# Optimization experiments

Measured on AMD Instinct MI355X. Metric: run time of the kernel, lower is better.

## Reference

```python
import jax, jax.numpy as jnp
import numpy as np

N, D, H1, K = 4096, 128, 256, 128


def setup_inputs() -> dict:
    key = jax.random.key(0)
    ks = jax.random.split(key, 8)
    A = jax.random.uniform(ks[3], (D, D), dtype=jnp.float32)
    A = A * (1.0 - jnp.eye(D, dtype=jnp.float32))  # DAG prob mask, no self-loops
    return {
        "x": jax.random.normal(ks[0], (N, D), dtype=jnp.float32),
        "weight": jax.random.normal(ks[1], (D, D), dtype=jnp.float32) * 0.1,
        "bias": jax.random.normal(ks[2], (1, D), dtype=jnp.float32) * 0.1,
        "A": A,
        "W1": jax.random.normal(ks[4], (D, H1), dtype=jnp.float32) * 0.1,
        "b1": jax.random.normal(ks[5], (H1,), dtype=jnp.float32) * 0.1,
        "W2": jax.random.normal(ks[6], (H1, K), dtype=jnp.float32) * 0.1,
        "b2": jax.random.normal(ks[7], (K,), dtype=jnp.float32) * 0.1,
    }


def reference(x, weight, bias, A, W1, b1, W2, b2):
    # to_adj (eval path): masked weights
    W = weight * A                                   # [D, D]
    y = x @ W + bias                                 # [N, D]
    # __expand__ builds diag(y[n]) [N,D,D]; since e[n,i,:] = y[n,i]*I[i,:],
    # the first Linear collapses to a per-row scaling of W1 (same math, fused):
    # e @ W1 -> y[n,i] * W1[i,:]
    h1 = jax.nn.relu(y[:, :, None] * W1[None, :, :] + b1)   # [N, D, H1]
    f = (h1 @ W2 + b2).sum(axis=2)                   # [N, D] (sum over output dim)
    # h_func, method='gnn'
    I = jnp.eye(D, dtype=x.dtype)
    A2 = jnp.square(W)
    M = I + A2 / D
    E = jnp.linalg.matrix_power(M, D - 1)
    h_val = (E.T * M).sum() - D
    # l1_reg (same prob mask in eval)
    reg = jnp.abs(W).sum()
    return (f, h_val, reg)
```

## Files before the change

### kernel.cpp

```cpp
#include <hip/hip_runtime.h>

#define NN 4096
#define DD 128
#define HH1 256

#define WS_S    0
#define WS_S2   16384
#define WS_S3   32768
#define WS_S4   49152
#define WS_W    65536
#define WS_W2S  81920
#define WS_PAIR 82176
#define WS_B2S  82688
#define WS_TACC 82696
#define WS_DONE 82708
#define WS_REGP 82712
#define WS_XT   82944
#define WS_YT   607232
#define WS_REQ_FLOATS 1131520
#define WS_REQ_BYTES  (WS_REQ_FLOATS * 4UL)

#define O_S    0
#define O_S2   16384
#define O_S3   32768
#define O_S4   49152
#define O_W2S  65536
#define O_B2S  65792
#define O_TACC 65808
#define O_DONE 65824
#define O_REGP 65840

__device__ __forceinline__ float waveReduce(float v) {
#pragma unroll
  for (int off = 32; off > 0; off >>= 1) v += __shfl_down(v, off, 64);
  return v;
}


__global__ __launch_bounds__(256) void kA2(
    const float* __restrict__ weight, const float* __restrict__ Amat,
    const float* __restrict__ W2, const float* __restrict__ b2,
    const float* __restrict__ b1v, const float* __restrict__ x,
    float* __restrict__ ws) {
  const int b = blockIdx.x, tid = threadIdx.x;
  __shared__ float s_lds[DD * DD];
  __shared__ float xs[128 * 133];
  if (b < 64) {
    const float4* w4 = (const float4*)weight;
    const float4* a4 = (const float4*)Amat;
    float4* s4 = (float4*)s_lds;
    const float inv = 1.0f / 128.0f;
    for (int e = tid; e < DD * DD / 4; e += 256) {
      float4 wv = w4[e], av = a4[e], o;
      float t;
      t = wv.x * av.x; o.x = t * t * inv;
      t = wv.y * av.y; o.y = t * t * inv;
      t = wv.z * av.z; o.z = t * t * inv;
      t = wv.w * av.w; o.w = t * t * inv;
      s4[e] = o;
    }
    __syncthreads();
    const int i = (b << 1) + (tid >> 7), j = tid & 127;
    const float* row = &s_lds[i * DD];
    float acc = 0.f;
#pragma unroll 8
    for (int k = 0; k < DD; ++k) acc = fmaf(row[k], s_lds[k * DD + j], acc);
    ws[WS_S2 + i * DD + j] = acc;
  } else if (b < 72) {
    const int base = (b - 64) * 2048;
    const float inv = 1.0f / 128.0f;
    for (int e = tid; e < 2048; e += 256) {
      const int idx = base + e;
      const float w = weight[idx] * Amat[idx];
      ws[WS_W + idx] = w;
      ws[WS_S + idx] = w * w * inv;
    }
  } else if (b == 72) {
    const float4* r = (const float4*)(W2 + tid * 128);
    float4 s4 = make_float4(0.f, 0.f, 0.f, 0.f);
#pragma unroll 8
    for (int k = 0; k < 32; ++k) {
      const float4 v = r[k];
      s4.x += v.x; s4.y += v.y; s4.z += v.z; s4.w += v.w;
    }
    const float w2sv = (s4.x + s4.y) + (s4.z + s4.w);
    ws[WS_W2S + tid] = w2sv;
    ((float2*)(ws + WS_PAIR))[tid] = make_float2(b1v[tid], w2sv);
  } else if (b == 73) {
    __shared__ float red[4];
    float v = (tid < 128) ? b2[tid] : 0.f;
    v = waveReduce(v);
    if ((tid & 63) == 0) red[tid >> 6] = v;
    __syncthreads();
    if (tid == 0) ws[WS_B2S] = (red[0] + red[1]) + (red[2] + red[3]);
    if (tid >= 64 && tid < 74) ws[WS_TACC + (tid - 64)] = 0.f;
    if (tid == 96) *(unsigned int*)(ws + WS_DONE) = 0u;
  } else if (b < 82) {
    const int bb = b - 74;
    const int base = bb * 2048;
    float s = 0.f;
    for (int e = tid; e < 2048; e += 256) {
      const int idx = base + e;
      s += fabsf(weight[idx] * Amat[idx]);
    }
    s = waveReduce(s);
    __shared__ float red2[4];
    if ((tid & 63) == 0) red2[tid >> 6] = s;
    __syncthreads();
    if (tid == 0) ws[WS_REGP + bb] = (red2[0] + red2[1]) + (red2[2] + red2[3]);
  } else {
    const int n0 = (b - 82) * 128;
    const float4* x4 = (const float4*)x;
    for (int e = tid; e < 4096; e += 256) {
      const int r = e >> 5, c = e & 31;
      const float4 v = x4[(n0 + r) * 32 + c];
      float* p = &xs[r * 133 + (c << 2)];
      p[0] = v.x; p[1] = v.y; p[2] = v.z; p[3] = v.w;
    }
    __syncthreads();
    float* xT = ws + WS_XT;
    const int c = tid & 31, ks = tid >> 5;
#pragma unroll 4
    for (int m = 0; m < 16; ++m) {
      const int k = ks + (m << 3);
      float4 o;
      o.x = xs[((c << 2) + 0) * 133 + k];
      o.y = xs[((c << 2) + 1) * 133 + k];
      o.z = xs[((c << 2) + 2) * 133 + k];
      o.w = xs[((c << 2) + 3) * 133 + k];
      *(float4*)&xT[k * NN + n0 + (c << 2)] = o;
    }
  }
}

__global__ __launch_bounds__(256) void kB2(const float* __restrict__ bias,
                                           float* __restrict__ ws) {
  const int tid = threadIdx.x;
  if (blockIdx.x < 128) {
    const int sb = blockIdx.x;
    const bool isS4 = sb >= 64;
    const int mb = isS4 ? sb - 64 : sb;
    const float* __restrict__ L = ws + WS_S2;
    const float* __restrict__ R = ws + (isS4 ? WS_S2 : WS_S);
    float* __restrict__ O = ws + (isS4 ? WS_S4 : WS_S3);
    const int i = (mb << 1) + (tid >> 7), j = tid & 127;
    float acc = 0.f;
#pragma unroll 8
    for (int k = 0; k < DD; ++k) acc = fmaf(L[i * DD + k], R[k * DD + j], acc);
    O[i * DD + j] = acc;
    return;
  }
  const int kb = blockIdx.x - 128;
  const int n0 = (kb & 15) << 8, i0 = (kb >> 4) << 3;
  const int n = n0 + tid;
  const float* __restrict__ xT = ws + WS_XT;
  const float* __restrict__ Wm = ws + WS_W;
  float* __restrict__ yT = ws + WS_YT;
  float acc[8];
#pragma unroll
  for (int q = 0; q < 8; ++q) acc[q] = 0.f;
#pragma unroll 8
  for (int k = 0; k < DD; ++k) {
    const float xv = xT[k * NN + n];
    const float* Wk = Wm + k * DD + i0;
#pragma unroll
    for (int q = 0; q < 8; ++q) acc[q] = fmaf(Wk[q], xv, acc[q]);
  }
#pragma unroll
  for (int q = 0; q < 8; ++q) yT[(i0 + q) * NN + n] = acc[q] + bias[i0 + q];
}

__global__ __launch_bounds__(256) void kC2(const float* __restrict__ W1,
                                           float* __restrict__ ws,
                                           float* __restrict__ out) {
  const int tid = threadIdx.x;
  if (blockIdx.x < 512) {
    __shared__ float ts[256 * 5];
    const int fb = blockIdx.x;
    const int n0 = (fb >> 5) << 8, i0 = (fb & 31) << 2;
    const int w = tid >> 6, l = tid & 63;
    const int iu = __builtin_amdgcn_readfirstlane(i0 + w);
    const float* __restrict__ yT = ws + WS_YT;
    float t[4];
#pragma unroll
    for (int q = 0; q < 4; ++q) t[q] = yT[iu * NN + n0 + (q << 6) + l];
    const float sb2 = ws[WS_B2S];
    float acc[4];
#pragma unroll
    for (int q = 0; q < 4; ++q) acc[q] = sb2;
    const float* __restrict__ W1row = W1 + iu * HH1;
    const float2* __restrict__ pr = (const float2*)(ws + WS_PAIR);
#pragma unroll 8
    for (int j = 0; j < HH1; ++j) {
      const float sw1 = W1row[j];
      const float2 p = pr[j];
      const float vb = p.x;
#pragma unroll
      for (int q = 0; q < 4; ++q) {
        const float h = fmaxf(fmaf(t[q], sw1, vb), 0.f);
        acc[q] = fmaf(h, p.y, acc[q]);
      }
    }
#pragma unroll
    for (int q = 0; q < 4; ++q) ts[((q << 6) + l) * 5 + w] = acc[q];
    __syncthreads();
    const int m = tid;
    float4 o;
    o.x = ts[m * 5 + 0]; o.y = ts[m * 5 + 1];
    o.z = ts[m * 5 + 2]; o.w = ts[m * 5 + 3];
    *(float4*)&out[(n0 + m) * DD + i0] = o;
    return;
  }
  const int tb = blockIdx.x - 512;
  const int i = (tb << 1) + (tid >> 7), j = tid & 127;
  const float* S1 = ws + WS_S;
  const float* S2 = ws + WS_S2;
  const float* S3 = ws + WS_S3;
  const float* S4 = ws + WS_S4;
  const float a1 = S1[i * DD + j], a2 = S2[i * DD + j], a3 = S3[i * DD + j];
  const float b1t = S1[j * DD + i], b2t = S2[j * DD + i],
              b3t = S3[j * DD + i], b4t = S4[j * DD + i];
  float e7 = 0.f;
#pragma unroll 8
  for (int k = 0; k < DD; ++k) e7 = fmaf(S3[i * DD + k], S4[k * DD + j], e7);
  float c[10];
  c[0] = a1 * b1t; c[1] = a2 * b1t; c[2] = a2 * b2t; c[3] = a3 * b2t;
  c[4] = a3 * b3t; c[5] = a3 * b4t; c[6] = e7 * b1t; c[7] = e7 * b2t;
  c[8] = e7 * b3t; c[9] = e7 * b4t;
  __shared__ float red[4][10];
#pragma unroll
  for (int m = 0; m < 10; ++m) {
    const float v = waveReduce(c[m]);
    if ((tid & 63) == 0) red[tid >> 6][m] = v;
  }
  __syncthreads();
  if (tid == 0) {
    float* tacc = ws + WS_TACC;
    for (int m = 0; m < 10; ++m)
      atomicAdd(&tacc[m], (red[0][m] + red[1][m]) + (red[2][m] + red[3][m]));
    __threadfence();
    unsigned int* done = (unsigned int*)(ws + WS_DONE);
    const unsigned int old = atomicAdd(done, 1u);
    if (old == 63u) {
      __threadfence();
      double h = 0.0, C = 8128.0;
      for (int kk = 2; kk <= 11; ++kk) {
        const float tv = atomicAdd(&tacc[kk - 2], 0.0f);
        h += C * (double)tv;
        C = C * (double)(128 - kk) / (double)(kk + 1);
      }
      float reg = 0.f;
      for (int m = 0; m < 8; ++m) reg += ws[WS_REGP + m];
      out[NN * DD] = (float)h;
      out[NN * DD + 1] = reg;
    }
  }
}

__global__ __launch_bounds__(256) void kA_old(
    const float* __restrict__ weight, const float* __restrict__ Amat,
    const float* __restrict__ W2, const float* __restrict__ b2,
    float* __restrict__ ws) {
  const int b = blockIdx.x, tid = threadIdx.x;
  if (b < 64) {
    __shared__ float s_lds[DD * DD];
    const float4* w4 = (const float4*)weight;
    const float4* a4 = (const float4*)Amat;
    float4* s4 = (float4*)s_lds;
    const float inv = 1.0f / 128.0f;
    for (int e = tid; e < DD * DD / 4; e += 256) {
      float4 wv = w4[e], av = a4[e], o;
      float t;
      t = wv.x * av.x; o.x = t * t * inv;
      t = wv.y * av.y; o.y = t * t * inv;
      t = wv.z * av.z; o.z = t * t * inv;
      t = wv.w * av.w; o.w = t * t * inv;
      s4[e] = o;
    }
    __syncthreads();
    const int i = (b << 1) + (tid >> 7), j = tid & 127;
    const float* row = &s_lds[i * DD];
    float acc = 0.f;
#pragma unroll 8
    for (int k = 0; k < DD; ++k) acc = fmaf(row[k], s_lds[k * DD + j], acc);
    ws[O_S2 + i * DD + j] = acc;
  } else if (b < 72) {
    const int base = (b - 64) * 2048;
    const float inv = 1.0f / 128.0f;
    for (int e = tid; e < 2048; e += 256) {
      const int idx = base + e;
      const float w = weight[idx] * Amat[idx];
      ws[O_S + idx] = w * w * inv;
    }
  } else if (b == 72) {
    const float4* r = (const float4*)(W2 + tid * 128);
    float4 s4 = make_float4(0.f, 0.f, 0.f, 0.f);
#pragma unroll 8
    for (int k = 0; k < 32; ++k) {
      const float4 v = r[k];
      s4.x += v.x; s4.y += v.y; s4.z += v.z; s4.w += v.w;
    }
    ws[O_W2S + tid] = (s4.x + s4.y) + (s4.z + s4.w);
  } else if (b == 73) {
    __shared__ float red[4];
    float v = (tid < 128) ? b2[tid] : 0.f;
    v = waveReduce(v);
    if ((tid & 63) == 0) red[tid >> 6] = v;
    __syncthreads();
    if (tid == 0) ws[O_B2S] = (red[0] + red[1]) + (red[2] + red[3]);
    if (tid >= 64 && tid < 74) ws[O_TACC + (tid - 64)] = 0.f;
    if (tid == 96) *(unsigned int*)(ws + O_DONE) = 0u;
  } else {
    const int bb = b - 74;
    const int base = bb * 2048;
    float s = 0.f;
    for (int e = tid; e < 2048; e += 256) {
      const int idx = base + e;
      s += fabsf(weight[idx] * Amat[idx]);
    }
    s = waveReduce(s);
    __shared__ float red[4];
    if ((tid & 63) == 0) red[tid >> 6] = s;
    __syncthreads();
    if (tid == 0) ws[O_REGP + bb] = (red[0] + red[1]) + (red[2] + red[3]);
  }
}

__global__ __launch_bounds__(256) void kB_old(
    const float* __restrict__ x, const float* __restrict__ weight,
    const float* __restrict__ Amat, const float* __restrict__ bias,
    const float* __restrict__ W1, const float* __restrict__ b1v,
    float* __restrict__ ws, float* __restrict__ out) {
  const int tid = threadIdx.x;
  if (blockIdx.x < 128) {
    const int sb = blockIdx.x;
    const bool isS4 = sb >= 64;
    const int mb = isS4 ? sb - 64 : sb;
    const float* __restrict__ L = ws + O_S2;
    const float* __restrict__ R = ws + (isS4 ? O_S2 : O_S);
    float* __restrict__ O = ws + (isS4 ? O_S4 : O_S3);
    const int i = (mb << 1) + (tid >> 7), j = tid & 127;
    float acc = 0.f;
#pragma unroll 8
    for (int k = 0; k < DD; ++k) acc = fmaf(L[i * DD + k], R[k * DD + j], acc);
    O[i * DD + j] = acc;
    return;
  }
  __shared__ float xs[64 * 132];
  __shared__ float4 fq[4 * 256];
  __shared__ float wcol[4 * 128];
  __shared__ float ts[64 * 5];
  const int fb = blockIdx.x - 128;
  const int i0 = (fb & 31) << 2, n0 = (fb >> 5) << 6;
  const float4* x4 = (const float4*)x;
  for (int e = tid; e < 64 * 32; e += 256) {
    const int r = e >> 5, c = e & 31;
    *(float4*)&xs[r * 132 + (c << 2)] = x4[(n0 + r) * 32 + c];
  }
  for (int e = tid; e < 512; e += 256) {
    const int w = e >> 7, k = e & 127;
    const int gi = k * DD + i0 + w;
    wcol[(w << 7) + k] = weight[gi] * Amat[gi];
  }
  const float* w2s = ws + O_W2S;
  for (int e = tid; e < 1024; e += 256) {
    const int w = e >> 8, j = e & 255;
    fq[(w << 8) + j] = make_float4(W1[(i0 + w) * HH1 + j], b1v[j], w2s[j], 0.f);
  }
  __syncthreads();
  const int w = tid >> 6, l = tid & 63;
  float t = bias[i0 + w];
  const float4* xr = (const float4*)&xs[l * 132];
  const float4* wc = (const float4*)&wcol[w << 7];
#pragma unroll
  for (int k = 0; k < 32; ++k) {
    const float4 xv = xr[k], wv = wc[k];
    t = fmaf(xv.x, wv.x, t);
    t = fmaf(xv.y, wv.y, t);
    t = fmaf(xv.z, wv.z, t);
    t = fmaf(xv.w, wv.w, t);
  }
  float acc = ws[O_B2S];
  const float4* fp = &fq[w << 8];
#pragma unroll 8
  for (int j = 0; j < HH1; ++j) {
    const float4 c = fp[j];
    acc = fmaf(fmaxf(fmaf(t, c.x, c.y), 0.f), c.z, acc);
  }
  ts[l * 5 + w] = acc;
  __syncthreads();
  if (tid < 64) {
    const float4 o = make_float4(ts[tid * 5 + 0], ts[tid * 5 + 1],
                                 ts[tid * 5 + 2], ts[tid * 5 + 3]);
    *(float4*)&out[(n0 + tid) * DD + i0] = o;
  }
}

__global__ __launch_bounds__(256) void kC_old(float* __restrict__ ws,
                                              float* __restrict__ out) {
  const int tid = threadIdx.x;
  const int i = (blockIdx.x << 1) + (tid >> 7), j = tid & 127;
  const float* S1 = ws + O_S;
  const float* S2 = ws + O_S2;
  const float* S3 = ws + O_S3;
  const float* S4 = ws + O_S4;
  const float a1 = S1[i * DD + j], a2 = S2[i * DD + j], a3 = S3[i * DD + j];
  const float b1t = S1[j * DD + i], b2t = S2[j * DD + i],
              b3t = S3[j * DD + i], b4t = S4[j * DD + i];
  float e7 = 0.f;
#pragma unroll 8
  for (int k = 0; k < DD; ++k) e7 = fmaf(S3[i * DD + k], S4[k * DD + j], e7);
  float c[10];
  c[0] = a1 * b1t; c[1] = a2 * b1t; c[2] = a2 * b2t; c[3] = a3 * b2t;
  c[4] = a3 * b3t; c[5] = a3 * b4t; c[6] = e7 * b1t; c[7] = e7 * b2t;
  c[8] = e7 * b3t; c[9] = e7 * b4t;
  __shared__ float red[4][10];
#pragma unroll
  for (int m = 0; m < 10; ++m) {
    const float v = waveReduce(c[m]);
    if ((tid & 63) == 0) red[tid >> 6][m] = v;
  }
  __syncthreads();
  if (tid == 0) {
    float* tacc = ws + O_TACC;
    for (int m = 0; m < 10; ++m)
      atomicAdd(&tacc[m], (red[0][m] + red[1][m]) + (red[2][m] + red[3][m]));
    __threadfence();
    unsigned int* done = (unsigned int*)(ws + O_DONE);
    const unsigned int old = atomicAdd(done, 1u);
    if (old == 63u) {
      __threadfence();
      double h = 0.0, C = 8128.0;
      for (int kk = 2; kk <= 11; ++kk) {
        const float tv = atomicAdd(&tacc[kk - 2], 0.0f);
        h += C * (double)tv;
        C = C * (double)(128 - kk) / (double)(kk + 1);
      }
      float reg = 0.f;
      for (int m = 0; m < 8; ++m) reg += ws[O_REGP + m];
      out[NN * DD] = (float)h;
      out[NN * DD + 1] = reg;
    }
  }
}

extern "C" void kernel_launch(void* const* d_in, const int* in_sizes, int n_in,
                              void* d_out, int out_size, void* d_ws,
                              size_t ws_size, hipStream_t stream) {
  const float* x      = (const float*)d_in[0];
  const float* weight = (const float*)d_in[1];
  const float* bias   = (const float*)d_in[2];
  const float* Amat   = (const float*)d_in[3];
  const float* W1     = (const float*)d_in[4];
  const float* b1v    = (const float*)d_in[5];
  const float* W2     = (const float*)d_in[6];
  const float* b2     = (const float*)d_in[7];
  float* out = (float*)d_out;
  float* ws  = (float*)d_ws;

  if (ws_size >= WS_REQ_BYTES) {
    kA2<<<114, 256, 0, stream>>>(weight, Amat, W2, b2, b1v, x, ws);
    kB2<<<384, 256, 0, stream>>>(bias, ws);
    kC2<<<576, 256, 0, stream>>>(W1, ws, out);
  } else {
    kA_old<<<82, 256, 0, stream>>>(weight, Amat, W2, b2, ws);
    kB_old<<<128 + 2048, 256, 0, stream>>>(x, weight, Amat, bias, W1, b1v, ws,
                                           out);
    kC_old<<<64, 256, 0, stream>>>(ws, out);
  }
}
```

Before: 107.5 us.

## Replace per-element hidden-layer loop with sorted-breakpoint piecewise-linear lookup

For each input feature i, f(t) is a sum of ReLUs in the scalar t, so it is piecewise linear. The new kB2 blocks compute each ReLU's breakpoint, bitonic-sort them in shared memory, and prefix-sum the slope and intercept contributions into a table for each feature. kC2 then replaces the 256-step FMA/max loop per output with a binary search over the breakpoints and a single FMA. This removes most of the arithmetic in the f stage but adds sorting and scan work, extra workspace, and a risk of small rounding differences near breakpoints.

After: 110.8 us. +3.1%, slower.

```diff
diff --git a/kernel.cpp b/kernel.cpp
--- a/kernel.cpp
+++ b/kernel.cpp
@@ -17,7 +17,9 @@
 #define WS_REGP 82712
 #define WS_XT   82944
 #define WS_YT   607232
-#define WS_REQ_FLOATS 1131520
+#define WS_BP   1131520
+#define WS_AB   1164288
+#define WS_REQ_FLOATS 1230080
 #define WS_REQ_BYTES  (WS_REQ_FLOATS * 4UL)
 
 #define O_S    0
@@ -134,8 +136,12 @@
 }
 
 __global__ __launch_bounds__(256) void kB2(const float* __restrict__ bias,
+                                           const float* __restrict__ W1,
                                            float* __restrict__ ws) {
   const int tid = threadIdx.x;
+  __shared__ float sk[256];
+  __shared__ int   si[256];
+  __shared__ float s0[256], s1[256], s2[256], s3[256];
   if (blockIdx.x < 128) {
     const int sb = blockIdx.x;
     const bool isS4 = sb >= 64;
@@ -150,65 +156,126 @@
     O[i * DD + j] = acc;
     return;
   }
-  const int kb = blockIdx.x - 128;
-  const int n0 = (kb & 15) << 8, i0 = (kb >> 4) << 3;
-  const int n = n0 + tid;
-  const float* __restrict__ xT = ws + WS_XT;
-  const float* __restrict__ Wm = ws + WS_W;
-  float* __restrict__ yT = ws + WS_YT;
-  float acc[8];
-#pragma unroll
-  for (int q = 0; q < 8; ++q) acc[q] = 0.f;
-#pragma unroll 8
-  for (int k = 0; k < DD; ++k) {
-    const float xv = xT[k * NN + n];
-    const float* Wk = Wm + k * DD + i0;
-#pragma unroll
-    for (int q = 0; q < 8; ++q) acc[q] = fmaf(Wk[q], xv, acc[q]);
-  }
-#pragma unroll
-  for (int q = 0; q < 8; ++q) yT[(i0 + q) * NN + n] = acc[q] + bias[i0 + q];
-}
-
-__global__ __launch_bounds__(256) void kC2(const float* __restrict__ W1,
-                                           float* __restrict__ ws,
+  if (blockIdx.x < 384) {
+    const int kb = blockIdx.x - 128;
+    const int n0 = (kb & 15) << 8, i0 = (kb >> 4) << 3;
+    const int n = n0 + tid;
+    const float* __restrict__ xT = ws + WS_XT;
+    const float* __restrict__ Wm = ws + WS_W;
+    float* __restrict__ yT = ws + WS_YT;
+    float acc[8];
+#pragma unroll
+    for (int q = 0; q < 8; ++q) acc[q] = 0.f;
+#pragma unroll 8
+    for (int k = 0; k < DD; ++k) {
+      const float xv = xT[k * NN + n];
+      const float* Wk = Wm + k * DD + i0;
+#pragma unroll
+      for (int q = 0; q < 8; ++q) acc[q] = fmaf(Wk[q], xv, acc[q]);
+    }
+#pragma unroll
+    for (int q = 0; q < 8; ++q) yT[(i0 + q) * NN + n] = acc[q] + bias[i0 + q];
+    return;
+  }
+  const int i = blockIdx.x - 384;
+  const float2* pr = (const float2*)(ws + WS_PAIR);
+  const int j = tid;
+  {
+    const float w1 = W1[i * HH1 + j];
+    const float2 p = pr[j];
+    float bp, da, dc, na, nc;
+    if (w1 > 0.f) {
+      const float a = w1 * p.y, c = p.x * p.y;
+      bp = -p.x / w1; da = a; dc = c; na = 0.f; nc = 0.f;
+    } else if (w1 < 0.f) {
+      const float a = w1 * p.y, c = p.x * p.y;
+      bp = -p.x / w1; da = -a; dc = -c; na = a; nc = c;
+    } else {
+      const float c = (p.x > 0.f) ? p.x * p.y : 0.f;
+      bp = 3.4e38f; da = 0.f; dc = -c; na = 0.f; nc = c;
+    }
+    sk[j] = bp; si[j] = j;
+    s0[j] = da; s1[j] = dc; s2[j] = na; s3[j] = nc;
+  }
+  __syncthreads();
+  for (int k = 2; k <= 256; k <<= 1) {
+    for (int jj = k >> 1; jj > 0; jj >>= 1) {
+      const int partner = tid ^ jj;
+      if (partner > tid) {
+        const float k0 = sk[tid], k1 = sk[partner];
+        const int   p0 = si[tid], p1 = si[partner];
+        const bool up = ((tid & k) == 0);
+        const bool sw = up ? (k0 > k1) : (k0 < k1);
+        if (sw) { sk[tid] = k1; sk[partner] = k0; si[tid] = p1; si[partner] = p0; }
+      }
+      __syncthreads();
+    }
+  }
+  {
+    const int jj = si[tid];
+    const float g0 = s0[jj], g1 = s1[jj], g2 = s2[jj], g3 = s3[jj];
+    __syncthreads();
+    s0[tid] = g0; s1[tid] = g1; s2[tid] = g2; s3[tid] = g3;
+    ws[WS_BP + i * 256 + tid] = sk[tid];
+  }
+  __syncthreads();
+  for (int d = 1; d < 256; d <<= 1) {
+    float a0 = s0[tid], a1 = s1[tid], a2 = s2[tid], a3 = s3[tid];
+    float b0 = 0.f, b1x = 0.f, b2x = 0.f, b3x = 0.f;
+    if (tid >= d) { b0 = s0[tid - d]; b1x = s1[tid - d]; b2x = s2[tid - d]; b3x = s3[tid - d]; }
+    __syncthreads();
+    s0[tid] = a0 + b0; s1[tid] = a1 + b1x; s2[tid] = a2 + b2x; s3[tid] = a3 + b3x;
+    __syncthreads();
+  }
+  {
+    const float ta = s2[255], tc = s3[255];
+    const float b2s = ws[WS_B2S];
+    const float ex0 = (tid > 0) ? s0[tid - 1] : 0.f;
+    const float ex1 = (tid > 0) ? s1[tid - 1] : 0.f;
+    float2* ab = ((float2*)(ws + WS_AB)) + i * 257;
+    ab[tid] = make_float2(ex0 + ta, ex1 + tc + b2s);
+    if (tid == 255) ab[256] = make_float2(s0[255] + ta, s1[255] + tc + b2s);
+  }
+}
+
+__global__ __launch_bounds__(256) void kC2(float* __restrict__ ws,
                                            float* __restrict__ out) {
   const int tid = threadIdx.x;
   if (blockIdx.x < 512) {
+    __shared__ float s_bp[4][256];
+    __shared__ float2 s_ab[4][257];
     __shared__ float ts[256 * 5];
     const int fb = blockIdx.x;
     const int n0 = (fb >> 5) << 8, i0 = (fb & 31) << 2;
+    for (int e = tid; e < 1024; e += 256) {
+      const int w = e >> 8, r = e & 255;
+      s_bp[w][r] = ws[WS_BP + (i0 + w) * 256 + r];
+    }
+    const float2* abws = (const float2*)(ws + WS_AB);
+#pragma unroll
+    for (int w = 0; w < 4; ++w)
+      for (int e = tid; e < 257; e += 256) s_ab[w][e] = abws[(i0 + w) * 257 + e];
+    __syncthreads();
     const int w = tid >> 6, l = tid & 63;
-    const int iu = __builtin_amdgcn_readfirstlane(i0 + w);
-    const float* __restrict__ yT = ws + WS_YT;
-    float t[4];
-#pragma unroll
-    for (int q = 0; q < 4; ++q) t[q] = yT[iu * NN + n0 + (q << 6) + l];
-    const float sb2 = ws[WS_B2S];
+    const float* yTb = ws + WS_YT + (i0 + w) * NN + n0 + l;
     float acc[4];
 #pragma unroll
-    for (int q = 0; q < 4; ++q) acc[q] = sb2;
-    const float* __restrict__ W1row = W1 + iu * HH1;
-    const float2* __restrict__ pr = (const float2*)(ws + WS_PAIR);
-#pragma unroll 8
-    for (int j = 0; j < HH1; ++j) {
-      const float sw1 = W1row[j];
-      const float2 p = pr[j];
-      const float vb = p.x;
-#pragma unroll
-      for (int q = 0; q < 4; ++q) {
-        const float h = fmaxf(fmaf(t[q], sw1, vb), 0.f);
-        acc[q] = fmaf(h, p.y, acc[q]);
-      }
+    for (int q = 0; q < 4; ++q) {
+      const float t = yTb[q << 6];
+      int r = 0;
+#pragma unroll
+      for (int st = 128; st >= 1; st >>= 1)
+        if (s_bp[w][r + st - 1] <= t) r += st;
+      const float2 ab = s_ab[w][r];
+      acc[q] = fmaf(ab.x, t, ab.y);
     }
 #pragma unroll
     for (int q = 0; q < 4; ++q) ts[((q << 6) + l) * 5 + w] = acc[q];
     __syncthreads();
-    const int m = tid;
     float4 o;
-    o.x = ts[m * 5 + 0]; o.y = ts[m * 5 + 1];
-    o.z = ts[m * 5 + 2]; o.w = ts[m * 5 + 3];
-    *(float4*)&out[(n0 + m) * DD + i0] = o;
+    o.x = ts[tid * 5 + 0]; o.y = ts[tid * 5 + 1];
+    o.z = ts[tid * 5 + 2]; o.w = ts[tid * 5 + 3];
+    *(float4*)&out[(n0 + tid) * DD + i0] = o;
     return;
   }
   const int tb = blockIdx.x - 512;
@@ -460,8 +527,8 @@
 
   if (ws_size >= WS_REQ_BYTES) {
     kA2<<<114, 256, 0, stream>>>(weight, Amat, W2, b2, b1v, x, ws);
-    kB2<<<384, 256, 0, stream>>>(bias, ws);
-    kC2<<<576, 256, 0, stream>>>(W1, ws, out);
+    kB2<<<512, 256, 0, stream>>>(bias, W1, ws);
+    kC2<<<576, 256, 0, stream>>>(ws, out);
   } else {
     kA_old<<<82, 256, 0, stream>>>(weight, Amat, W2, b2, ws);
     kB_old<<<128 + 2048, 256, 0, stream>>>(x, weight, Amat, bias, W1, b1v, ws,
```
